# Performance work log

Measured on AMD Instinct MI355X. Metric: run time of the kernel, lower is better.

The kernel has to match this reference:

```python
import jax, jax.numpy as jnp
import numpy as np
import math

B, S, D, H = 2, 2048, 1024, 16
HD = D // H  # head_dim = 64


def setup_inputs() -> dict:
    key = jax.random.key(0)
    k1, k2, k3, k4, k5 = jax.random.split(key, 5)
    scale_in = 1.0 / math.sqrt(D)
    return {
        "x": jax.random.normal(k1, (B, S, D), dtype=jnp.float32),
        "Wqkv": jax.random.normal(k2, (3 * D, D), dtype=jnp.float32) * scale_in,
        "bqkv": jax.random.normal(k3, (3 * D,), dtype=jnp.float32) * 0.01,
        "Wout": jax.random.normal(k4, (D, D), dtype=jnp.float32) * scale_in,
        "bout": jax.random.normal(k5, (D,), dtype=jnp.float32) * 0.01,
    }


def reference(x, Wqkv, bqkv, Wout, bout):
    Bs, Sl, Dm = x.shape
    # qkv projection: torch Linear is x @ W.T + b
    qkv = x @ Wqkv.T + bqkv                        # [B,S,3D]
    qkv = qkv.reshape(Bs, Sl, 3, H, HD)
    q, k, v = qkv[:, :, 0], qkv[:, :, 1], qkv[:, :, 2]  # each [B,S,H,d]
    softmax_scale = 1.0 / math.sqrt(HD)
    # NOTE: source einsum 'bshd,btjd->bsht' sums k over its head axis j.
    # Equivalent efficient form: pre-sum k (and v) over heads.
    k_sum = k.sum(axis=2)                          # [B,S,d]
    v_sum = v.sum(axis=2)                          # [B,S,d]
    scores = jnp.einsum('bshd,btd->bsht', q, k_sum) * softmax_scale  # [B,S,H,T]
    causal_mask = jnp.triu(jnp.ones((Sl, Sl), dtype=bool), k=1)      # [S,T]
    scores = jnp.where(causal_mask[None, :, None, :], -jnp.inf, scores)
    attn = jax.nn.softmax(scores, axis=-1)
    # dropout p=0.0 / eval mode -> identity
    out = jnp.einsum('bsht,btd->bshd', attn, v_sum)  # [B,S,H,d]
    out = out.reshape(Bs, Sl, Dm)
    return out @ Wout.T + bout
```

## Files before the change

### kernel.cpp

```cpp
#include <hip/hip_runtime.h>


#define S_LEN 2048
#define DIM 1024

using floatx4 = __attribute__((ext_vector_type(4))) float;
using halfx8  = __attribute__((ext_vector_type(8))) _Float16;
using halfx4  = __attribute__((ext_vector_type(4))) _Float16;
using halfx2  = __attribute__((ext_vector_type(2))) _Float16;
using fp16x2  = __attribute__((ext_vector_type(2))) __fp16;

__device__ __forceinline__ floatx4 mfma16(halfx8 a, halfx8 b, floatx4 c) {
  return __builtin_amdgcn_mfma_f32_16x16x32_f16(a, b, c, 0, 0, 0);
}

__device__ __forceinline__ void gll16(const void* g, void* l) {
  __builtin_amdgcn_global_load_lds(
      (const __attribute__((address_space(1))) void*)g,
      (__attribute__((address_space(3))) void*)l, 16, 0, 0);
}

__global__ __launch_bounds__(256) void prep_all(
    const float* __restrict__ x, const float* __restrict__ wqkv,
    const float* __restrict__ bqkv, const float* __restrict__ wout,
    _Float16* __restrict__ xb, _Float16* __restrict__ wcomb,
    _Float16* __restrict__ woutb, float* __restrict__ bcomb) {
  int bx = blockIdx.x;
  if (bx < 6144) {
    size_t i4 = ((size_t)bx * 256 + threadIdx.x) * 4;
    const float* src;
    _Float16* dst;
    size_t off;
    if (i4 < 4194304) { src = x; dst = xb; off = i4; }
    else if (i4 < 5242880) { src = wqkv; dst = wcomb; off = i4 - 4194304; }
    else { src = wout; dst = woutb; off = i4 - 5242880; }
    float4 v = *(const float4*)(src + off);
    halfx4 o;
    o[0] = (_Float16)v.x; o[1] = (_Float16)v.y;
    o[2] = (_Float16)v.z; o[3] = (_Float16)v.w;
    *(halfx4*)(dst + off) = o;
  } else {
    int gid = (bx - 6144) * 256 + threadIdx.x;
    int c = gid >> 10, j = gid & 1023;
    int row0 = (c < 64) ? (1024 + c) : (2048 + c - 64);
    float s = 0.f;
#pragma unroll
    for (int h = 0; h < 16; ++h) s += wqkv[(size_t)(row0 + h * 64) * 1024 + j];
    wcomb[(size_t)1024 * 1024 + gid] = (_Float16)s;
    if (gid < 1024) bcomb[gid] = bqkv[gid];
    if (gid < 128) {
      int b0 = (gid < 64) ? (1024 + gid) : (2048 + gid - 64);
      float sb = 0.f;
#pragma unroll
      for (int h = 0; h < 16; ++h) sb += bqkv[b0 + h * 64];
      bcomb[1024 + gid] = sb;
    }
  }
}

template <int MODE>
__global__ __launch_bounds__(256, 6) void gemm_t5(
    const _Float16* __restrict__ A, const _Float16* __restrict__ W,
    const float* __restrict__ bias, void* __restrict__ Cv,
    _Float16* __restrict__ kbo, _Float16* __restrict__ vto) {
  const int K = 1024;
  __shared__ _Float16 As[64][64];
  __shared__ _Float16 Ws[64][64];
  int tid = threadIdx.x;
  int lane = tid & 63, w = tid >> 6, ln = lane & 15, q4 = lane >> 4;
  int m0 = blockIdx.x * 64, n0 = blockIdx.y * 64;
  int rr = lane >> 3, gg = ((lane & 7) ^ rr) * 8;
  const _Float16* agp = A + (size_t)(m0 + w * 16 + rr) * K + gg;
  const _Float16* wgp = W + (size_t)(n0 + w * 16 + rr) * K + gg;
  floatx4 acc[4] = {};
  for (int kt = 0; kt < K; kt += 64) {
    __syncthreads();
    gll16(agp + kt, &As[w * 16][0]);
    gll16(agp + (size_t)8 * K + kt, &As[w * 16 + 8][0]);
    gll16(wgp + kt, &Ws[w * 16][0]);
    gll16(wgp + (size_t)8 * K + kt, &Ws[w * 16 + 8][0]);
    __syncthreads();
#pragma unroll
    for (int kh = 0; kh < 2; ++kh) {
      int sw = ((q4 + 4 * kh) ^ (ln & 7)) * 8;
      halfx8 bf = *(const halfx8*)&Ws[w * 16 + ln][sw];
#pragma unroll
      for (int mf = 0; mf < 4; ++mf) {
        halfx8 af = *(const halfx8*)&As[mf * 16 + ln][sw];
        acc[mf] = mfma16(af, bf, acc[mf]);
      }
    }
  }
  const float qscale = 0.18033688011112042f;
  int col = n0 + w * 16 + ln;
  float bv = bias[col];
  if constexpr (MODE == 1) {
#pragma unroll
    for (int mf = 0; mf < 4; ++mf)
#pragma unroll
      for (int i = 0; i < 4; ++i) {
        int row = m0 + mf * 16 + q4 * 4 + i;
        ((float*)Cv)[(size_t)row * 1024 + col] = acc[mf][i] + bv;
      }
  } else {
    if (col < 1024) {
#pragma unroll
      for (int mf = 0; mf < 4; ++mf)
#pragma unroll
        for (int i = 0; i < 4; ++i) {
          int row = m0 + mf * 16 + q4 * 4 + i;
          ((_Float16*)Cv)[(size_t)row * 1024 + col] =
              (_Float16)((acc[mf][i] + bv) * qscale);
        }
    } else if (col < 1088) {
      int ck = col - 1024;
#pragma unroll
      for (int mf = 0; mf < 4; ++mf)
#pragma unroll
        for (int i = 0; i < 4; ++i) {
          int row = m0 + mf * 16 + q4 * 4 + i;
          kbo[(size_t)row * 64 + ck] = (_Float16)(acc[mf][i] + bv);
        }
    } else {
      int d = col - 1088;
#pragma unroll
      for (int mf = 0; mf < 4; ++mf) {
        int row0 = m0 + mf * 16 + q4 * 4;
        int bb = row0 >> 11, sps = row0 & 2047;
        int blk = sps & ~127, tl = sps & 127;
        int p0 = (tl >> 6) * 64 + ((tl >> 2) & 3) * 8 + ((tl >> 4) & 3) * 2;
        _Float16* basep = &vto[((size_t)((bb << 6) + d)) * S_LEN + blk];
        halfx2 lo, hi;
        lo[0] = (_Float16)(acc[mf][0] + bv);
        lo[1] = (_Float16)(acc[mf][1] + bv);
        hi[0] = (_Float16)(acc[mf][2] + bv);
        hi[1] = (_Float16)(acc[mf][3] + bv);
        *(halfx2*)&basep[p0] = lo;
        *(halfx2*)&basep[p0 + 32] = hi;
      }
    }
  }
}

__global__ __launch_bounds__(256, 4) void flash_attn15(
    const _Float16* __restrict__ Qb, const _Float16* __restrict__ kb,
    const _Float16* __restrict__ vtb, _Float16* __restrict__ aob) {
  __shared__ _Float16 Ks[128][64];
  __shared__ _Float16 Vt[64][128];
  int tid = threadIdx.x;
  int lane = tid & 63, w = tid >> 6, ln = lane & 15, q4 = lane >> 4;
  int bx = (int)blockIdx.x;
  int q = bx >> 8, lo = bx & 255;
  int b = lo & 1, p = lo >> 1;
  int crow = (q == 0) ? p : (q == 1) ? (255 - p) : (q == 2) ? (256 + p)
                                                            : (511 - p);
  int s0 = crow * 4;
  int s = s0 + w;
  size_t bS = (size_t)b * S_LEN;

  int rr = lane >> 3, ggk = ((lane & 7) ^ rr) * 8;
  const _Float16* kgp = kb + (bS + w * 32 + rr) * 64 + ggk;
  int vr = lane >> 4;
  int vhalf = (lane >> 3) & 1, vg = lane & 7;
  const _Float16* vgp[4];
#pragma unroll
  for (int j = 0; j < 4; ++j) {
    int row = w * 16 + 4 * j + vr;
    vgp[j] = vtb + ((size_t)b * 64 + row) * S_LEN + vhalf * 64 +
             ((vg ^ (row & 7)) * 8);
  }
  int swk0 = (q4 ^ (ln & 7)) * 8;
  int swk1 = ((q4 + 4) ^ (ln & 7)) * 8;

  const _Float16* qp = Qb + (bS + s) * DIM + ln * 64 + q4 * 8;
  halfx8 bq0 = *(const halfx8*)qp, bq1 = *(const halfx8*)(qp + 32);

  float m_run = -1e30f, l_run = 0.f;
  floatx4 oacc[4] = {};
  int nt = (crow >> 5) + 1;

  for (int it = 0; it < nt; ++it) {
    int t0 = it << 7;
    __syncthreads();
#pragma unroll
    for (int j = 0; j < 4; ++j)
      gll16(kgp + (size_t)(t0 + 8 * j) * 64, &Ks[w * 32 + 8 * j][0]);
#pragma unroll
    for (int j = 0; j < 4; ++j)
      gll16(vgp[j] + t0, &Vt[w * 16 + 4 * j][0]);
    __syncthreads();

    floatx4 sf[2][4];
    __builtin_amdgcn_s_setprio(1);
#pragma unroll
    for (int tq = 0; tq < 2; ++tq)
#pragma unroll
      for (int tf = 0; tf < 4; ++tf) {
        halfx8 ak0 = *(const halfx8*)&Ks[tq * 64 + tf * 16 + ln][swk0];
        halfx8 ak1 = *(const halfx8*)&Ks[tq * 64 + tf * 16 + ln][swk1];
        floatx4 z = {};
        z = mfma16(ak0, bq0, z);
        sf[tq][tf] = mfma16(ak1, bq1, z);
      }
    __builtin_amdgcn_s_setprio(0);
    if (it == nt - 1) {
#pragma unroll
      for (int tq = 0; tq < 2; ++tq)
#pragma unroll
        for (int tf = 0; tf < 4; ++tf)
#pragma unroll
          for (int i = 0; i < 4; ++i) {
            int t = t0 + tq * 64 + tf * 16 + q4 * 4 + i;
            if (t > s) sf[tq][tf][i] = -1e30f;
          }
    }
    float tm = -1e30f;
#pragma unroll
    for (int tq = 0; tq < 2; ++tq)
#pragma unroll
      for (int tf = 0; tf < 4; ++tf)
        tm = fmaxf(tm, fmaxf(fmaxf(sf[tq][tf][0], sf[tq][tf][1]),
                             fmaxf(sf[tq][tf][2], sf[tq][tf][3])));
    tm = fmaxf(tm, __shfl_xor(tm, 16));
    tm = fmaxf(tm, __shfl_xor(tm, 32));
    if (!__all(tm <= m_run + 8.f)) {
      float mn = fmaxf(m_run, tm);
      float alpha = exp2f(m_run - mn);
      m_run = mn;
      l_run *= alpha;
#pragma unroll
      for (int n2 = 0; n2 < 4; ++n2)
#pragma unroll
        for (int i = 0; i < 4; ++i) oacc[n2][i] *= alpha;
    }
    float rs = 0.f;
    unsigned bpw[4][4];
#pragma unroll
    for (int tq = 0; tq < 2; ++tq)
#pragma unroll
      for (int tf = 0; tf < 4; ++tf) {
        float p0 = exp2f(sf[tq][tf][0] - m_run);
        float p1 = exp2f(sf[tq][tf][1] - m_run);
        float p2 = exp2f(sf[tq][tf][2] - m_run);
        float p3 = exp2f(sf[tq][tf][3] - m_run);
        rs += (p0 + p1) + (p2 + p3);
        union { fp16x2 h; unsigned u; } c0, c1;
        c0.h = __builtin_amdgcn_cvt_pkrtz(p0, p1);
        c1.h = __builtin_amdgcn_cvt_pkrtz(p2, p3);
        bpw[2 * tq][tf] = c0.u;
        bpw[2 * tq + 1][tf] = c1.u;
      }
    rs += __shfl_xor(rs, 16);
    rs += __shfl_xor(rs, 32);
    l_run += rs;
    __builtin_amdgcn_s_setprio(1);
#pragma unroll
    for (int kc = 0; kc < 4; ++kc) {
      union { unsigned u[4]; halfx8 v; } bpu;
#pragma unroll
      for (int ww = 0; ww < 4; ++ww) bpu.u[ww] = bpw[kc][ww];
      int half = (kc >> 1) * 64;
      int sw = ((q4 + 4 * (kc & 1)) ^ (ln & 7)) * 8;
#pragma unroll
      for (int n2 = 0; n2 < 4; ++n2) {
        halfx8 av = *(const halfx8*)&Vt[n2 * 16 + ln][half + sw];
        oacc[n2] = mfma16(av, bpu.v, oacc[n2]);
      }
    }
    __builtin_amdgcn_s_setprio(0);
  }
  float inv = 1.0f / l_run;
#pragma unroll
  for (int n2 = 0; n2 < 4; ++n2) {
    halfx4 o;
#pragma unroll
    for (int i = 0; i < 4; ++i) o[i] = (_Float16)(oacc[n2][i] * inv);
    *(halfx4*)(aob + (bS + s) * DIM + ln * 64 + n2 * 16 + q4 * 4) = o;
  }
}

extern "C" void kernel_launch(void* const* d_in, const int* in_sizes, int n_in,
                              void* d_out, int out_size, void* d_ws,
                              size_t ws_size, hipStream_t stream) {
  const float* x    = (const float*)d_in[0];
  const float* wqkv = (const float*)d_in[1];
  const float* bqkv = (const float*)d_in[2];
  const float* wout = (const float*)d_in[3];
  const float* bout = (const float*)d_in[4];
  float* out = (float*)d_out;
  char* ws = (char*)d_ws;
  _Float16* xb    = (_Float16*)(ws);
  _Float16* qb    = (_Float16*)(ws + (8u << 20));
  _Float16* aob   = (_Float16*)(ws + (16u << 20));
  _Float16* kb    = (_Float16*)(ws + (24u << 20));
  _Float16* vtb   = (_Float16*)(ws + (24u << 20) + (512u << 10));
  _Float16* wcomb = (_Float16*)(ws + (25u << 20));
  _Float16* woutb = (_Float16*)(ws + (27u << 20) + (512u << 10));
  float*    bcomb = (float*)(ws + (29u << 20) + (512u << 10));

  hipLaunchKernelGGL(prep_all, dim3(6656), dim3(256), 0, stream,
                     x, wqkv, bqkv, wout, xb, wcomb, woutb, bcomb);
  hipLaunchKernelGGL((gemm_t5<0>), dim3(64, 18), dim3(256), 0, stream,
                     xb, wcomb, bcomb, (void*)qb, kb, vtb);
  hipLaunchKernelGGL(flash_attn15, dim3(1024), dim3(256), 0, stream,
                     qb, kb, vtb, aob);
  hipLaunchKernelGGL((gemm_t5<1>), dim3(64, 16), dim3(256), 0, stream,
                     aob, woutb, bout, (void*)out, nullptr, nullptr);
}
```

Before: 157.2 us.

## Drop LDS staging in attention and read K/V directly per wave

Rewrites the attention kernel so each wave loads its K and V fragments straight from global memory (and cache) instead of staging 128-key tiles in shared memory, which removes both block-wide barriers per tile. Each wave now handles two query rows, s and S-1-s, to balance the causal work, and launches half as many blocks with a lower occupancy bound. The trade-off is that the four waves in a block no longer share tile loads, so each wave issues its own global reads. Those reads now expose memory latency directly rather than being amortised through shared memory.

```diff
diff --git a/kernel.cpp b/kernel.cpp
--- a/kernel.cpp
+++ b/kernel.cpp
@@ -142,140 +142,118 @@
   }
 }
 
-__global__ __launch_bounds__(256, 4) void flash_attn15(
+__global__ __launch_bounds__(256, 2) void flash_attn16(
     const _Float16* __restrict__ Qb, const _Float16* __restrict__ kb,
     const _Float16* __restrict__ vtb, _Float16* __restrict__ aob) {
-  __shared__ _Float16 Ks[128][64];
-  __shared__ _Float16 Vt[64][128];
   int tid = threadIdx.x;
   int lane = tid & 63, w = tid >> 6, ln = lane & 15, q4 = lane >> 4;
-  int bx = (int)blockIdx.x;
-  int q = bx >> 8, lo = bx & 255;
-  int b = lo & 1, p = lo >> 1;
-  int crow = (q == 0) ? p : (q == 1) ? (255 - p) : (q == 2) ? (256 + p)
-                                                            : (511 - p);
-  int s0 = crow * 4;
-  int s = s0 + w;
+  int gw = (int)blockIdx.x * 4 + w;
+  int b = gw & 1, sh = gw >> 1;
   size_t bS = (size_t)b * S_LEN;
-
-  int rr = lane >> 3, ggk = ((lane & 7) ^ rr) * 8;
-  const _Float16* kgp = kb + (bS + w * 32 + rr) * 64 + ggk;
-  int vr = lane >> 4;
-  int vhalf = (lane >> 3) & 1, vg = lane & 7;
-  const _Float16* vgp[4];
-#pragma unroll
-  for (int j = 0; j < 4; ++j) {
-    int row = w * 16 + 4 * j + vr;
-    vgp[j] = vtb + ((size_t)b * 64 + row) * S_LEN + vhalf * 64 +
-             ((vg ^ (row & 7)) * 8);
-  }
-  int swk0 = (q4 ^ (ln & 7)) * 8;
-  int swk1 = ((q4 + 4) ^ (ln & 7)) * 8;
-
-  const _Float16* qp = Qb + (bS + s) * DIM + ln * 64 + q4 * 8;
-  halfx8 bq0 = *(const halfx8*)qp, bq1 = *(const halfx8*)(qp + 32);
-
-  float m_run = -1e30f, l_run = 0.f;
-  floatx4 oacc[4] = {};
-  int nt = (crow >> 5) + 1;
-
-  for (int it = 0; it < nt; ++it) {
-    int t0 = it << 7;
-    __syncthreads();
-#pragma unroll
-    for (int j = 0; j < 4; ++j)
-      gll16(kgp + (size_t)(t0 + 8 * j) * 64, &Ks[w * 32 + 8 * j][0]);
-#pragma unroll
-    for (int j = 0; j < 4; ++j)
-      gll16(vgp[j] + t0, &Vt[w * 16 + 4 * j][0]);
-    __syncthreads();
-
-    floatx4 sf[2][4];
-    __builtin_amdgcn_s_setprio(1);
-#pragma unroll
-    for (int tq = 0; tq < 2; ++tq)
-#pragma unroll
-      for (int tf = 0; tf < 4; ++tf) {
-        halfx8 ak0 = *(const halfx8*)&Ks[tq * 64 + tf * 16 + ln][swk0];
-        halfx8 ak1 = *(const halfx8*)&Ks[tq * 64 + tf * 16 + ln][swk1];
-        floatx4 z = {};
-        z = mfma16(ak0, bq0, z);
-        sf[tq][tf] = mfma16(ak1, bq1, z);
-      }
-    __builtin_amdgcn_s_setprio(0);
-    if (it == nt - 1) {
+  const _Float16* kbase = kb + bS * 64;
+  const _Float16* vbase = vtb + (size_t)b * 64 * S_LEN;
+
+#pragma unroll 1
+  for (int pass = 0; pass < 2; ++pass) {
+    int s = pass ? (S_LEN - 1 - sh) : sh;
+    const _Float16* qp = Qb + (bS + s) * DIM + ln * 64 + q4 * 8;
+    halfx8 bq0 = *(const halfx8*)qp, bq1 = *(const halfx8*)(qp + 32);
+
+    float m_run = -1e30f, l_run = 0.f;
+    floatx4 oacc[4] = {};
+    int nt = (s >> 7) + 1;
+
+    for (int it = 0; it < nt; ++it) {
+      int t0 = it << 7;
+      floatx4 sf[2][4];
+      __builtin_amdgcn_s_setprio(1);
 #pragma unroll
       for (int tq = 0; tq < 2; ++tq)
 #pragma unroll
+        for (int tf = 0; tf < 4; ++tf) {
+          const _Float16* kp =
+              kbase + (size_t)(t0 + tq * 64 + tf * 16 + ln) * 64 + q4 * 8;
+          halfx8 ak0 = *(const halfx8*)kp;
+          halfx8 ak1 = *(const halfx8*)(kp + 32);
+          floatx4 z = {};
+          z = mfma16(ak0, bq0, z);
+          sf[tq][tf] = mfma16(ak1, bq1, z);
+        }
+      __builtin_amdgcn_s_setprio(0);
+      if (it == nt - 1) {
+#pragma unroll
+        for (int tq = 0; tq < 2; ++tq)
+#pragma unroll
+          for (int tf = 0; tf < 4; ++tf)
+#pragma unroll
+            for (int i = 0; i < 4; ++i) {
+              int t = t0 + tq * 64 + tf * 16 + q4 * 4 + i;
+              if (t > s) sf[tq][tf][i] = -1e30f;
+            }
+      }
+      float tm = -1e30f;
+#pragma unroll
+      for (int tq = 0; tq < 2; ++tq)
+#pragma unroll
         for (int tf = 0; tf < 4; ++tf)
-#pragma unroll
-          for (int i = 0; i < 4; ++i) {
-            int t = t0 + tq * 64 + tf * 16 + q4 * 4 + i;
-            if (t > s) sf[tq][tf][i] = -1e30f;
-          }
-    }
-    float tm = -1e30f;
-#pragma unroll
-    for (int tq = 0; tq < 2; ++tq)
-#pragma unroll
-      for (int tf = 0; tf < 4; ++tf)
-        tm = fmaxf(tm, fmaxf(fmaxf(sf[tq][tf][0], sf[tq][tf][1]),
-                             fmaxf(sf[tq][tf][2], sf[tq][tf][3])));
-    tm = fmaxf(tm, __shfl_xor(tm, 16));
-    tm = fmaxf(tm, __shfl_xor(tm, 32));
-    if (!__all(tm <= m_run + 8.f)) {
-      float mn = fmaxf(m_run, tm);
-      float alpha = exp2f(m_run - mn);
-      m_run = mn;
-      l_run *= alpha;
-#pragma unroll
-      for (int n2 = 0; n2 < 4; ++n2)
-#pragma unroll
-        for (int i = 0; i < 4; ++i) oacc[n2][i] *= alpha;
-    }
-    float rs = 0.f;
-    unsigned bpw[4][4];
-#pragma unroll
-    for (int tq = 0; tq < 2; ++tq)
-#pragma unroll
-      for (int tf = 0; tf < 4; ++tf) {
-        float p0 = exp2f(sf[tq][tf][0] - m_run);
-        float p1 = exp2f(sf[tq][tf][1] - m_run);
-        float p2 = exp2f(sf[tq][tf][2] - m_run);
-        float p3 = exp2f(sf[tq][tf][3] - m_run);
-        rs += (p0 + p1) + (p2 + p3);
-        union { fp16x2 h; unsigned u; } c0, c1;
-        c0.h = __builtin_amdgcn_cvt_pkrtz(p0, p1);
-        c1.h = __builtin_amdgcn_cvt_pkrtz(p2, p3);
-        bpw[2 * tq][tf] = c0.u;
-        bpw[2 * tq + 1][tf] = c1.u;
-      }
-    rs += __shfl_xor(rs, 16);
-    rs += __shfl_xor(rs, 32);
-    l_run += rs;
-    __builtin_amdgcn_s_setprio(1);
-#pragma unroll
-    for (int kc = 0; kc < 4; ++kc) {
-      union { unsigned u[4]; halfx8 v; } bpu;
-#pragma unroll
-      for (int ww = 0; ww < 4; ++ww) bpu.u[ww] = bpw[kc][ww];
-      int half = (kc >> 1) * 64;
-      int sw = ((q4 + 4 * (kc & 1)) ^ (ln & 7)) * 8;
-#pragma unroll
-      for (int n2 = 0; n2 < 4; ++n2) {
-        halfx8 av = *(const halfx8*)&Vt[n2 * 16 + ln][half + sw];
-        oacc[n2] = mfma16(av, bpu.v, oacc[n2]);
-      }
-    }
-    __builtin_amdgcn_s_setprio(0);
-  }
-  float inv = 1.0f / l_run;
-#pragma unroll
-  for (int n2 = 0; n2 < 4; ++n2) {
-    halfx4 o;
-#pragma unroll
-    for (int i = 0; i < 4; ++i) o[i] = (_Float16)(oacc[n2][i] * inv);
-    *(halfx4*)(aob + (bS + s) * DIM + ln * 64 + n2 * 16 + q4 * 4) = o;
+          tm = fmaxf(tm, fmaxf(fmaxf(sf[tq][tf][0], sf[tq][tf][1]),
+                               fmaxf(sf[tq][tf][2], sf[tq][tf][3])));
+      tm = fmaxf(tm, __shfl_xor(tm, 16));
+      tm = fmaxf(tm, __shfl_xor(tm, 32));
+      if (!__all(tm <= m_run + 8.f)) {
+        float mn = fmaxf(m_run, tm);
+        float alpha = exp2f(m_run - mn);
+        m_run = mn;
+        l_run *= alpha;
+#pragma unroll
+        for (int n2 = 0; n2 < 4; ++n2)
+#pragma unroll
+          for (int i = 0; i < 4; ++i) oacc[n2][i] *= alpha;
+      }
+      float rs = 0.f;
+      unsigned bpw[4][4];
+#pragma unroll
+      for (int tq = 0; tq < 2; ++tq)
+#pragma unroll
+        for (int tf = 0; tf < 4; ++tf) {
+          float p0 = exp2f(sf[tq][tf][0] - m_run);
+          float p1 = exp2f(sf[tq][tf][1] - m_run);
+          float p2 = exp2f(sf[tq][tf][2] - m_run);
+          float p3 = exp2f(sf[tq][tf][3] - m_run);
+          rs += (p0 + p1) + (p2 + p3);
+          union { fp16x2 h; unsigned u; } c0, c1;
+          c0.h = __builtin_amdgcn_cvt_pkrtz(p0, p1);
+          c1.h = __builtin_amdgcn_cvt_pkrtz(p2, p3);
+          bpw[2 * tq][tf] = c0.u;
+          bpw[2 * tq + 1][tf] = c1.u;
+        }
+      rs += __shfl_xor(rs, 16);
+      rs += __shfl_xor(rs, 32);
+      l_run += rs;
+      __builtin_amdgcn_s_setprio(1);
+#pragma unroll
+      for (int kc = 0; kc < 4; ++kc) {
+        union { unsigned u[4]; halfx8 v; } bpu;
+#pragma unroll
+        for (int ww = 0; ww < 4; ++ww) bpu.u[ww] = bpw[kc][ww];
+#pragma unroll
+        for (int n2 = 0; n2 < 4; ++n2) {
+          const _Float16* vp = vbase + (size_t)(n2 * 16 + ln) * S_LEN + t0 +
+                               kc * 32 + q4 * 8;
+          halfx8 av = *(const halfx8*)vp;
+          oacc[n2] = mfma16(av, bpu.v, oacc[n2]);
+        }
+      }
+      __builtin_amdgcn_s_setprio(0);
+    }
+    float inv = 1.0f / l_run;
+#pragma unroll
+    for (int n2 = 0; n2 < 4; ++n2) {
+      halfx4 o;
+#pragma unroll
+      for (int i = 0; i < 4; ++i) o[i] = (_Float16)(oacc[n2][i] * inv);
+      *(halfx4*)(aob + (bS + s) * DIM + ln * 64 + n2 * 16 + q4 * 4) = o;
+    }
   }
 }
 
@@ -302,7 +280,7 @@
                      x, wqkv, bqkv, wout, xb, wcomb, woutb, bcomb);
   hipLaunchKernelGGL((gemm_t5<0>), dim3(64, 18), dim3(256), 0, stream,
                      xb, wcomb, bcomb, (void*)qb, kb, vtb);
-  hipLaunchKernelGGL(flash_attn15, dim3(1024), dim3(256), 0, stream,
+  hipLaunchKernelGGL(flash_attn16, dim3(512), dim3(256), 0, stream,
                      qb, kb, vtb, aob);
   hipLaunchKernelGGL((gemm_t5<1>), dim3(64, 16), dim3(256), 0, stream,
                      aob, woutb, bout, (void*)out, nullptr, nullptr);
```

After: 237.6 us. 51.2% more time.
